# Performance work log

Measured on AMD Instinct MI355X. Metric: run time of the kernel, lower is better.

The kernel has to match this reference:

```python
import jax, jax.numpy as jnp
import numpy as np

B, L, H, E = 8, 1024, 8, 64
HIST = 512


def setup_inputs() -> dict:
    key = jax.random.key(0)
    ks = jax.random.split(key, 6)
    shp = (B, L, H, E)
    q, k, v, qd, kd, vd = (jax.random.normal(kk, shp, dtype=jnp.float32) for kk in ks)
    # DoubleTriangularCausalMask surrogate: strictly-upper-triangular causal mask (diagonal=1)
    attn_mask = jnp.triu(jnp.ones((L, L), dtype=bool), k=1)[None, None]  # (1,1,L,S)
    return {
        "queries": q, "keys": k, "values": v,
        "queries_drawn": qd, "keys_drawn": kd, "values_drawn": vd,
        "attn_mask": attn_mask, "history_len": HIST,
    }


def reference(queries, keys, values, queries_drawn, keys_drawn, values_drawn, attn_mask, history_len):
    # drawn_y=True branch of FullFixedTimeCausalConstructiveAttention with history_len set.
    B, L, H, E = queries.shape
    scale = 1.0 / float(np.sqrt(E))
    hist = history_len
    idx = jnp.arange(hist, L)

    # queries[:, hist:] = queries_drawn[:, hist:]
    q_eff = jnp.concatenate([queries[:, :hist], queries_drawn[:, hist:]], axis=1)

    scores = jnp.einsum('blhe,bshe->bhls', q_eff, keys)  # (B,H,L,S)
    # diagonal positions l>=hist use drawn keys: q_eff[l] . keys_drawn[l]
    diag_scores = jnp.einsum('blhe,blhe->bhl', q_eff[:, hist:], keys_drawn[:, hist:])
    scores = scores.at[:, :, idx, idx].set(diag_scores)

    scores = jnp.where(attn_mask, -jnp.inf, scores)
    A = jax.nn.softmax(scale * scores, axis=-1)  # (B,H,L,S); dropout rate 0 in eval

    # values substitution on the diagonal (l==s, l>=hist) is a rank-1 correction;
    # avoids materializing the torch (B,H,D,L,S) repeated tensor.
    V = jnp.einsum('bhls,bshd->blhd', A, values)
    diag_A = A[:, :, idx, idx]                      # (B,H,L-hist)
    delta = values_drawn[:, hist:] - values[:, hist:]  # (B,L-hist,H,D)
    V = V.at[:, hist:].add(jnp.transpose(diag_A, (0, 2, 1))[..., None] * delta)
    return V
```

## Files before the change

kernel.cpp:

```cpp
#include <hip/hip_runtime.h>

#define LL   1024
#define HH   8
#define EE   64
#define KSTR 72

#define SCALE2 0.18033688011112043f

typedef _Float16 f16;
typedef _Float16 v8h  __attribute__((ext_vector_type(8)));
typedef _Float16 h2   __attribute__((ext_vector_type(2)));
typedef float    v4f  __attribute__((ext_vector_type(4)));
typedef int      v2i  __attribute__((ext_vector_type(2)));

__device__ __forceinline__ float fexp2(float x) {
#if __has_builtin(__builtin_amdgcn_exp2f)
  return __builtin_amdgcn_exp2f(x);
#else
  return __expf(x * 0.6931471805599453f);
#endif
}

__device__ __forceinline__ h2 pkh2(float a, float b) {
#if __has_builtin(__builtin_amdgcn_cvt_pkrtz)
  return __builtin_bit_cast(h2, __builtin_amdgcn_cvt_pkrtz(a, b));
#else
  h2 r; r[0] = (f16)a; r[1] = (f16)b; return r;
#endif
}

__device__ __forceinline__ float red4max(float x) {
#if __has_builtin(__builtin_amdgcn_permlane16_swap) && __has_builtin(__builtin_amdgcn_permlane32_swap)
  int xi = __float_as_int(x);
  v2i a = __builtin_amdgcn_permlane16_swap(xi, xi, false, false);
  float m = fmaxf(__int_as_float(a.x), __int_as_float(a.y));
  int mi = __float_as_int(m);
  v2i b = __builtin_amdgcn_permlane32_swap(mi, mi, false, false);
  return fmaxf(__int_as_float(b.x), __int_as_float(b.y));
#else
  x = fmaxf(x, __shfl_xor(x, 16));
  return fmaxf(x, __shfl_xor(x, 32));
#endif
}

__device__ __forceinline__ float red4sum(float x) {
#if __has_builtin(__builtin_amdgcn_permlane16_swap) && __has_builtin(__builtin_amdgcn_permlane32_swap)
  int xi = __float_as_int(x);
  v2i a = __builtin_amdgcn_permlane16_swap(xi, xi, false, false);
  float s = __int_as_float(a.x) + __int_as_float(a.y);
  int si = __float_as_int(s);
  v2i b = __builtin_amdgcn_permlane32_swap(si, si, false, false);
  return __int_as_float(b.x) + __int_as_float(b.y);
#else
  x += __shfl_xor(x, 16);
  return x + __shfl_xor(x, 32);
#endif
}

__device__ __forceinline__ void load16f(const float* __restrict__ p, float* __restrict__ f) {
  const float4* p4 = reinterpret_cast<const float4*>(p);
  float4 a = p4[0], b = p4[1], c = p4[2], d = p4[3];
  f[0]=a.x;  f[1]=a.y;  f[2]=a.z;  f[3]=a.w;
  f[4]=b.x;  f[5]=b.y;  f[6]=b.z;  f[7]=b.w;
  f[8]=c.x;  f[9]=c.y;  f[10]=c.z; f[11]=c.w;
  f[12]=d.x; f[13]=d.y; f[14]=d.z; f[15]=d.w;
}

__device__ __forceinline__ void load8f(const float* __restrict__ p, float* __restrict__ f) {
  const float4* p4 = reinterpret_cast<const float4*>(p);
  float4 a = p4[0], b = p4[1];
  f[0]=a.x; f[1]=a.y; f[2]=a.z; f[3]=a.w;
  f[4]=b.x; f[5]=b.y; f[6]=b.z; f[7]=b.w;
}

struct TileState {
  v4f   o[4];
  float m, l, pd;
};

__device__ __forceinline__ void tile_update(
    TileState& st, const v8h* __restrict__ qf, bool dt, bool drawn,
    const f16* __restrict__ Ks, const f16* __restrict__ Vt,
    const float* __restrict__ zd,
    int w, int ln, int lq,
    const int* __restrict__ rk, const int* __restrict__ kb)
{
  v4f S[4];
#pragma unroll
  for (int nb = 0; nb < 4; ++nb) {
    const f16* krow = &Ks[rk[nb] * KSTR + 8 * lq];
    v8h k0 = *reinterpret_cast<const v8h*>(krow);
    v8h k1 = *reinterpret_cast<const v8h*>(krow + 32);
    v4f acc = (v4f){0.f, 0.f, 0.f, 0.f};
    acc = __builtin_amdgcn_mfma_f32_16x16x32_f16(k0, qf[0], acc, 0, 0, 0);
    acc = __builtin_amdgcn_mfma_f32_16x16x32_f16(k1, qf[1], acc, 0, 0, 0);
    S[nb] = acc;
  }

  float z[4][4];
#pragma unroll
  for (int nb = 0; nb < 4; ++nb)
#pragma unroll
    for (int r = 0; r < 4; ++r) z[nb][r] = S[nb][r] * SCALE2;

  const int qlocal = w * 16 + ln;
  if (dt) {
    const float zdq = drawn ? zd[qlocal] : 0.f;
#pragma unroll
    for (int nb = 0; nb < 4; ++nb) {
#pragma unroll
      for (int r = 0; r < 4; ++r) {
        const int kl = kb[nb] + r;
        if (kl > qlocal)                 z[nb][r] = -1e30f;
        else if (drawn && kl == qlocal)  z[nb][r] = zdq;
      }
    }
  }

  float a0 = fmaxf(fmaxf(z[0][0], z[0][1]), fmaxf(z[0][2], z[0][3]));
  float a1 = fmaxf(fmaxf(z[1][0], z[1][1]), fmaxf(z[1][2], z[1][3]));
  float a2 = fmaxf(fmaxf(z[2][0], z[2][1]), fmaxf(z[2][2], z[2][3]));
  float a3 = fmaxf(fmaxf(z[3][0], z[3][1]), fmaxf(z[3][2], z[3][3]));
  const float mx = red4max(fmaxf(fmaxf(a0, a1), fmaxf(a2, a3)));

  const float mn = fmaxf(st.m, mx);
  const float al = fexp2(st.m - mn);
  st.m = mn;

  float p[4][4], rsum = 0.f, pdl = 0.f;
#pragma unroll
  for (int nb = 0; nb < 4; ++nb) {
#pragma unroll
    for (int r = 0; r < 4; ++r) {
      const float pv = fexp2(z[nb][r] - mn);
      p[nb][r] = pv;
      rsum += pv;
      if (dt && drawn && (kb[nb] + r) == qlocal) pdl = pv;
    }
  }
  rsum = red4sum(rsum);
  if (dt && drawn) st.pd = red4sum(pdl);
  st.l = st.l * al + rsum;
#pragma unroll
  for (int nb = 0; nb < 4; ++nb)
#pragma unroll
    for (int r = 0; r < 4; ++r) st.o[nb][r] *= al;

  h2 wq[4][2];
#pragma unroll
  for (int nb = 0; nb < 4; ++nb) {
    wq[nb][0] = pkh2(p[nb][0], p[nb][1]);
    wq[nb][1] = pkh2(p[nb][2], p[nb][3]);
  }
  const bool swp = (lq & 1);
  union U8 { v8h v; h2 h[4]; } A0, A1;
  A0.h[0] = swp ? wq[1][0] : wq[0][0];
  A0.h[1] = swp ? wq[1][1] : wq[0][1];
  A0.h[2] = swp ? wq[0][0] : wq[1][0];
  A0.h[3] = swp ? wq[0][1] : wq[1][1];
  A1.h[0] = swp ? wq[3][0] : wq[2][0];
  A1.h[1] = swp ? wq[3][1] : wq[2][1];
  A1.h[2] = swp ? wq[2][0] : wq[3][0];
  A1.h[3] = swp ? wq[2][1] : wq[3][1];

#pragma unroll
  for (int nb = 0; nb < 4; ++nb) {
    const int d   = nb * 16 + ln;
    const int dsw = (d >> 3) & 7;
    const f16* vbase = &Vt[d * KSTR];
    v8h v0 = *reinterpret_cast<const v8h*>(vbase + (((lq    ) ^ dsw) & 7) * 8);
    v8h v1 = *reinterpret_cast<const v8h*>(vbase + (((lq + 4) ^ dsw) & 7) * 8);
    st.o[nb] = __builtin_amdgcn_mfma_f32_16x16x32_f16(v0, A0.v, st.o[nb], 0, 0, 0);
    st.o[nb] = __builtin_amdgcn_mfma_f32_16x16x32_f16(v1, A1.v, st.o[nb], 0, 0, 0);
  }
}

extern "C" __global__ __launch_bounds__(256, 4)
void ftcca_split(const float* __restrict__ Q,  const float* __restrict__ K,
                 const float* __restrict__ V,  const float* __restrict__ Qd,
                 const float* __restrict__ Kd, const float* __restrict__ Vd,
                 float* __restrict__ out)
{
  __shared__ f16   Ks[64 * KSTR];
  __shared__ f16   Vt[64 * KSTR];
  __shared__ float zdiag[64];

  const int bh  = blockIdx.x & 63;
  const int a   = blockIdx.x >> 6;
  const int qt  = 15 - a;
  const bool drawn = (qt >= 8);
  const int b   = bh >> 3, h = bh & 7;
  const int t   = threadIdx.x;
  const int w    = t >> 6;
  const int lane = t & 63;
  const int ln   = lane & 15;
  const int lq   = lane >> 4;
  const int rs   = t >> 2;
  const int es0  = (t & 3) * 16;
  const int vr0  = (t >> 3) * 2;
  const int vd0  = (t & 7) * 8;

  const size_t base = ((size_t)b * LL * HH + h) * EE;
  const int ROWF = HH * EE;

  const int q2 = ln >> 2;
  int rk[4], kb[4];
  rk[0] = ln + ((q2 + 1) >> 1) * 8;
  rk[1] = ln + 4 + (q2 >> 1) * 8;
  rk[2] = rk[0] + 32;
  rk[3] = rk[1] + 32;
  kb[0] = 4 * lq + ((lq + 1) >> 1) * 8;
  kb[1] = 4 * lq + 4 + (lq >> 1) * 8;
  kb[2] = kb[0] + 32;
  kb[3] = kb[1] + 32;

  if (drawn) {
    const int l = qt * 64 + rs;
    const float* qrow = Qd + base + (size_t)l * ROWF + es0;
    const float* krow = Kd + base + (size_t)l * ROWF + es0;
    float par = 0.f;
#pragma unroll
    for (int i = 0; i < 16; ++i) par += qrow[i] * krow[i];
    par += __shfl_xor(par, 1);
    par += __shfl_xor(par, 2);
    if ((t & 3) == 0) zdiag[rs] = SCALE2 * par;
  }

  const int rowt_q = w * 16 + ln;
  const float* qsrc = drawn ? Qd : Q;
  v8h qf[2];
  {
    const float* pq = qsrc + base + (size_t)(qt * 64 + rowt_q) * ROWF;
#pragma unroll
    for (int c = 0; c < 2; ++c) {
      const float* x = pq + 32 * c + 8 * lq;
#pragma unroll
      for (int j = 0; j < 8; ++j) qf[c][j] = (f16)x[j];
    }
  }

  TileState st;
#pragma unroll
  for (int nb = 0; nb < 4; ++nb) st.o[nb] = (v4f){0, 0, 0, 0};
  st.m = -1e30f; st.l = 0.f; st.pd = 0.f;

  float tk[16], tv[16];
  load16f(K + base + (size_t)rs * ROWF + es0, tk);
  load8f(V + base + (size_t)vr0 * ROWF + vd0, tv);
  load8f(V + base + (size_t)(vr0 + 1) * ROWF + vd0, tv + 8);

  for (int i = 0; i <= qt; ++i) {
    __syncthreads();
    {
      v8h k0, k1;
#pragma unroll
      for (int j = 0; j < 8; ++j) { k0[j] = (f16)tk[j]; k1[j] = (f16)tk[8 + j]; }
      v8h* kd0 = reinterpret_cast<v8h*>(&Ks[rs * KSTR + es0]);
      kd0[0] = k0;
      kd0[1] = k1;
      const int vswz = vr0 >> 3;
#pragma unroll
      for (int dd = 0; dd < 8; ++dd) {
        const int d  = vd0 + dd;
        const int ch = (vswz ^ (d >> 3)) & 7;
        h2 val; val[0] = (f16)tv[dd]; val[1] = (f16)tv[8 + dd];
        *reinterpret_cast<h2*>(&Vt[d * KSTR + ch * 8 + (vr0 & 7)]) = val;
      }
    }
    __syncthreads();

    if (i < qt) {
      const size_t r0 = (size_t)((i + 1) * 64);
      load16f(K + base + (r0 + rs) * ROWF + es0, tk);
      load8f(V + base + (r0 + vr0) * ROWF + vd0, tv);
      load8f(V + base + (r0 + vr0 + 1) * ROWF + vd0, tv + 8);
    }

    tile_update(st, qf, i == qt, drawn, Ks, Vt, zdiag, w, ln, lq, rk, kb);
  }

  const float inv = 1.f / st.l;
  const float pdinv = st.pd * inv;
  const int lrow = qt * 64 + w * 16 + ln;

#pragma unroll
  for (int nb = 0; nb < 4; ++nb) {
    const int d0 = nb * 16 + lq * 4;
    const size_t g = base + (size_t)lrow * ROWF + d0;
    float4 o4;
    o4.x = st.o[nb][0] * inv;
    o4.y = st.o[nb][1] * inv;
    o4.z = st.o[nb][2] * inv;
    o4.w = st.o[nb][3] * inv;
    if (drawn) {
      float4 vd4 = *reinterpret_cast<const float4*>(Vd + g);
      float4 v4  = *reinterpret_cast<const float4*>(V + g);
      o4.x += pdinv * (vd4.x - v4.x);
      o4.y += pdinv * (vd4.y - v4.y);
      o4.z += pdinv * (vd4.z - v4.z);
      o4.w += pdinv * (vd4.w - v4.w);
    }
    *reinterpret_cast<float4*>(out + g) = o4;
  }
}

extern "C" void kernel_launch(void* const* d_in, const int* in_sizes, int n_in,
                              void* d_out, int out_size, void* d_ws, size_t ws_size,
                              hipStream_t stream) {
  const float* q  = (const float*)d_in[0];
  const float* k  = (const float*)d_in[1];
  const float* v  = (const float*)d_in[2];
  const float* qd = (const float*)d_in[3];
  const float* kd = (const float*)d_in[4];
  const float* vd = (const float*)d_in[5];
  float* out = (float*)d_out;

  ftcca_split<<<dim3(1024), dim3(256), 0, stream>>>(q, k, v, qd, kd, vd, out);
}
```

Before: 155.5 us.

## Split long causal query tiles across two blocks with atomic-flag merge

The eight longest query tiles per batch-head are now split into two key-range halves processed by separate blocks, which stage partial outputs, row max, row sum and diagonal weight in a workspace. The second block to finish, detected via an atomic counter, merges both halves with log-sum-exp rescaling and applies the drawn-value correction. This is meant to even out the triangular causal workload and fill more of the GPU, and occupancy hints are raised. In exchange it adds a memset, workspace traffic, fences, and a per-tile merge step.

```diff
diff --git a/kernel.cpp b/kernel.cpp
--- a/kernel.cpp
+++ b/kernel.cpp
@@ -4,6 +4,8 @@
 #define HH   8
 #define EE   64
 #define KSTR 72
+#define PSTR 4352
+#define PBASE 1024
 
 #define SCALE2 0.18033688011112043f
 
@@ -175,20 +177,25 @@
   }
 }
 
-extern "C" __global__ __launch_bounds__(256, 4)
-void ftcca_split(const float* __restrict__ Q,  const float* __restrict__ K,
-                 const float* __restrict__ V,  const float* __restrict__ Qd,
-                 const float* __restrict__ Kd, const float* __restrict__ Vd,
-                 float* __restrict__ out)
+extern "C" __global__ __launch_bounds__(256, 8)
+void ftcca_sk(const float* __restrict__ Q,  const float* __restrict__ K,
+              const float* __restrict__ V,  const float* __restrict__ Qd,
+              const float* __restrict__ Kd, const float* __restrict__ Vd,
+              float* __restrict__ ws,       float* __restrict__ out)
 {
   __shared__ f16   Ks[64 * KSTR];
   __shared__ f16   Vt[64 * KSTR];
   __shared__ float zdiag[64];
-
-  const int bh  = blockIdx.x & 63;
-  const int a   = blockIdx.x >> 6;
-  const int qt  = 15 - a;
-  const bool drawn = (qt >= 8);
+  __shared__ int   oldflag;
+
+  const int g   = blockIdx.x;
+  const int bh  = g & 63;
+  const int u   = g >> 6;
+  int qt, s;
+  if (u < 16) { qt = 15 - (u >> 1); s = u & 1; }
+  else        { qt = 23 - u;        s = -1;    }
+  const bool split = (s >= 0);
+  const bool drawn = split;
   const int b   = bh >> 3, h = bh & 7;
   const int t   = threadIdx.x;
   const int w    = t >> 6;
@@ -203,6 +210,10 @@
   const size_t base = ((size_t)b * LL * HH + h) * EE;
   const int ROWF = HH * EE;
 
+  const int n  = qt + 1;
+  const int i0 = (s == 1) ? (n >> 1) : 0;
+  const int i1 = (s == 0) ? (n >> 1) : n;
+
   const int q2 = ln >> 2;
   int rk[4], kb[4];
   rk[0] = ln + ((q2 + 1) >> 1) * 8;
@@ -214,7 +225,7 @@
   kb[2] = kb[0] + 32;
   kb[3] = kb[1] + 32;
 
-  if (drawn) {
+  if (s == 1) {
     const int l = qt * 64 + rs;
     const float* qrow = Qd + base + (size_t)l * ROWF + es0;
     const float* krow = Kd + base + (size_t)l * ROWF + es0;
@@ -226,11 +237,11 @@
     if ((t & 3) == 0) zdiag[rs] = SCALE2 * par;
   }
 
-  const int rowt_q = w * 16 + ln;
+  const int qlocal = w * 16 + ln;
   const float* qsrc = drawn ? Qd : Q;
   v8h qf[2];
   {
-    const float* pq = qsrc + base + (size_t)(qt * 64 + rowt_q) * ROWF;
+    const float* pq = qsrc + base + (size_t)(qt * 64 + qlocal) * ROWF;
 #pragma unroll
     for (int c = 0; c < 2; ++c) {
       const float* x = pq + 32 * c + 8 * lq;
@@ -245,11 +256,11 @@
   st.m = -1e30f; st.l = 0.f; st.pd = 0.f;
 
   float tk[16], tv[16];
-  load16f(K + base + (size_t)rs * ROWF + es0, tk);
-  load8f(V + base + (size_t)vr0 * ROWF + vd0, tv);
-  load8f(V + base + (size_t)(vr0 + 1) * ROWF + vd0, tv + 8);
-
-  for (int i = 0; i <= qt; ++i) {
+  load16f(K + base + (size_t)(i0 * 64 + rs) * ROWF + es0, tk);
+  load8f(V + base + (size_t)(i0 * 64 + vr0) * ROWF + vd0, tv);
+  load8f(V + base + (size_t)(i0 * 64 + vr0 + 1) * ROWF + vd0, tv + 8);
+
+  for (int i = i0; i < i1; ++i) {
     __syncthreads();
     {
       v8h k0, k1;
@@ -269,7 +280,7 @@
     }
     __syncthreads();
 
-    if (i < qt) {
+    if (i + 1 < i1) {
       const size_t r0 = (size_t)((i + 1) * 64);
       load16f(K + base + (r0 + rs) * ROWF + es0, tk);
       load8f(V + base + (r0 + vr0) * ROWF + vd0, tv);
@@ -279,28 +290,71 @@
     tile_update(st, qf, i == qt, drawn, Ks, Vt, zdiag, w, ln, lq, rk, kb);
   }
 
-  const float inv = 1.f / st.l;
-  const float pdinv = st.pd * inv;
-  const int lrow = qt * 64 + w * 16 + ln;
+  const int lrow = qt * 64 + qlocal;
+
+  if (!split) {
+    const float inv = 1.f / st.l;
+#pragma unroll
+    for (int nb = 0; nb < 4; ++nb) {
+      const int d0 = nb * 16 + lq * 4;
+      const size_t gaddr = base + (size_t)lrow * ROWF + d0;
+      float4 o4;
+      o4.x = st.o[nb][0] * inv;
+      o4.y = st.o[nb][1] * inv;
+      o4.z = st.o[nb][2] * inv;
+      o4.w = st.o[nb][3] * inv;
+      *reinterpret_cast<float4*>(out + gaddr) = o4;
+    }
+    return;
+  }
+
+  const int pair = (bh << 3) + (qt - 8);
+  {
+    float* Pm = ws + PBASE + (size_t)(pair * 2 + s) * PSTR;
+#pragma unroll
+    for (int nb = 0; nb < 4; ++nb) {
+      float4 o4;
+      o4.x = st.o[nb][0]; o4.y = st.o[nb][1]; o4.z = st.o[nb][2]; o4.w = st.o[nb][3];
+      *reinterpret_cast<float4*>(&Pm[qlocal * 64 + nb * 16 + lq * 4]) = o4;
+    }
+    if (lq == 0) {
+      Pm[4096 + qlocal] = st.m;
+      Pm[4160 + qlocal] = st.l;
+      Pm[4224 + qlocal] = st.pd;
+    }
+  }
+  __threadfence();
+  __syncthreads();
+  if (t == 0) oldflag = atomicAdd(reinterpret_cast<int*>(ws) + pair, 1);
+  __syncthreads();
+  if (oldflag == 0) return;
+
+  __threadfence();
+  const float* Pp = ws + PBASE + (size_t)(pair * 2 + (s ^ 1)) * PSTR;
+  const float mb  = Pp[4096 + qlocal];
+  const float lb  = Pp[4160 + qlocal];
+  const float pdb = Pp[4224 + qlocal];
+
+  const float mm = fmaxf(st.m, mb);
+  const float ea = fexp2(st.m - mm);
+  const float eb = fexp2(mb - mm);
+  const float lt = st.l * ea + lb * eb;
+  const float inv = 1.f / lt;
+  const float pdinv = (st.pd * ea + pdb * eb) * inv;
 
 #pragma unroll
   for (int nb = 0; nb < 4; ++nb) {
     const int d0 = nb * 16 + lq * 4;
-    const size_t g = base + (size_t)lrow * ROWF + d0;
+    const size_t gaddr = base + (size_t)lrow * ROWF + d0;
+    float4 ob = *reinterpret_cast<const float4*>(&Pp[qlocal * 64 + nb * 16 + lq * 4]);
+    float4 vd4 = *reinterpret_cast<const float4*>(Vd + gaddr);
+    float4 v4  = *reinterpret_cast<const float4*>(V + gaddr);
     float4 o4;
-    o4.x = st.o[nb][0] * inv;
-    o4.y = st.o[nb][1] * inv;
-    o4.z = st.o[nb][2] * inv;
-    o4.w = st.o[nb][3] * inv;
-    if (drawn) {
-      float4 vd4 = *reinterpret_cast<const float4*>(Vd + g);
-      float4 v4  = *reinterpret_cast<const float4*>(V + g);
-      o4.x += pdinv * (vd4.x - v4.x);
-      o4.y += pdinv * (vd4.y - v4.y);
-      o4.z += pdinv * (vd4.z - v4.z);
-      o4.w += pdinv * (vd4.w - v4.w);
-    }
-    *reinterpret_cast<float4*>(out + g) = o4;
+    o4.x = (st.o[nb][0] * ea + ob.x * eb) * inv + pdinv * (vd4.x - v4.x);
+    o4.y = (st.o[nb][1] * ea + ob.y * eb) * inv + pdinv * (vd4.y - v4.y);
+    o4.z = (st.o[nb][2] * ea + ob.z * eb) * inv + pdinv * (vd4.z - v4.z);
+    o4.w = (st.o[nb][3] * ea + ob.w * eb) * inv + pdinv * (vd4.w - v4.w);
+    *reinterpret_cast<float4*>(out + gaddr) = o4;
   }
 }
 
@@ -314,6 +368,9 @@
   const float* kd = (const float*)d_in[4];
   const float* vd = (const float*)d_in[5];
   float* out = (float*)d_out;
-
-  ftcca_split<<<dim3(1024), dim3(256), 0, stream>>>(q, k, v, qd, kd, vd, out);
-}
+  float* ws  = (float*)d_ws;
+
+  hipMemsetAsync(d_ws, 0, 4096, stream);
+
+  ftcca_sk<<<dim3(1536), dim3(256), 0, stream>>>(q, k, v, qd, kd, vd, ws, out);
+}
```

After: 506.5 us. 3.26x slower.
